# Performance work log

Hardware: AMD Instinct MI355X
Metric: run time of the kernel (lower is better)

## Reference

```python
import jax, jax.numpy as jnp
import numpy as np

N_NODES = 50000
N_EDGES = 800000
F_IN = 128
HID = 128
N_GRAPHS = 64
N_CLASSES = 40


def _seg_max(vals, idx, num_segments):
    out = jax.ops.segment_max(vals, idx, num_segments=num_segments)
    # PyG max-aggregation fills empty segments with 0
    return jnp.where(jnp.isfinite(out), out, jnp.zeros_like(out))


def _mr_conv(x, src, dst, W, b):
    # message: x_j - x_i gathered per edge; aggregate: scatter-max at dst
    diff = x[src] - x[dst]                      # [E, F]
    aggr = _seg_max(diff, dst, x.shape[0])      # [N, F]
    return jnp.concatenate([x, aggr], axis=-1) @ W + b


def setup_inputs() -> dict:
    key = jax.random.key(0)
    ks = jax.random.split(key, 16)
    x = jax.random.normal(ks[0], (N_NODES, F_IN), dtype=jnp.float32)
    edge_index = jax.random.randint(ks[1], (2, N_EDGES), 0, N_NODES, dtype=jnp.int64) if jax.config.jax_enable_x64 else jax.random.randint(ks[1], (2, N_EDGES), 0, N_NODES).astype(jnp.int32)
    batch = jnp.sort(jax.random.randint(ks[2], (N_NODES,), 0, N_GRAPHS)).astype(jnp.int32)
    def lin(k, fan_in, fan_out):
        bound = 1.0 / np.sqrt(fan_in)
        kw, kb = jax.random.split(k)
        W = jax.random.uniform(kw, (fan_in, fan_out), minval=-bound, maxval=bound, dtype=jnp.float32)
        b = jax.random.uniform(kb, (fan_out,), minval=-bound, maxval=bound, dtype=jnp.float32)
        return W, b
    W1, b1 = lin(ks[3], 2 * F_IN, HID)
    W2, b2 = lin(ks[4], 2 * HID, HID)
    W3, b3 = lin(ks[5], 2 * HID, HID)
    Wf1, bf1 = lin(ks[6], HID, 64)
    Wf2, bf2 = lin(ks[7], 64, N_CLASSES)
    return {"x": x, "edge_index": edge_index, "batch": batch,
            "W1": W1, "b1": b1, "W2": W2, "b2": b2, "W3": W3, "b3": b3,
            "Wf1": Wf1, "bf1": bf1, "Wf2": Wf2, "bf2": bf2}


def reference(x, edge_index, batch, W1, b1, W2, b2, W3, b3, Wf1, bf1, Wf2, bf2):
    src, dst = edge_index[0], edge_index[1]
    # to_undirected: add reversed edges (dedup unnecessary: max is idempotent)
    src_u = jnp.concatenate([src, dst])
    dst_u = jnp.concatenate([dst, src])
    h = _mr_conv(x, src_u, dst_u, W1, b1)
    h = jax.nn.relu(h)
    h = _mr_conv(h, src_u, dst_u, W2, b2)
    h = jax.nn.relu(h)
    h = _mr_conv(h, src_u, dst_u, W3, b3)
    h = jax.nn.relu(h)
    g = _seg_max(h, batch, N_GRAPHS)            # global_max_pool -> [G, HID]
    g = jax.nn.relu(g @ Wf1 + bf1) @ Wf2 + bf2
    return jax.nn.log_softmax(g, axis=1)
```

## Files before the change

### kernel.cpp

```cpp
#include <hip/hip_runtime.h>
#include <hip/hip_bf16.h>
#include <math.h>

#define NODES 50000
#define FEAT 128
#define NB 196
#define BCAP 12288

typedef __attribute__((ext_vector_type(4))) float f32x4;
typedef __attribute__((ext_vector_type(8))) short short8;
union UV { uint4 u; short8 s; };

__device__ __forceinline__ unsigned bf16rne(float x) {
  unsigned u = __float_as_uint(x);
  return (u + 0x7FFFu + ((u >> 16) & 1u)) >> 16;
}

__global__ void k_zero(int* __restrict__ p, int n) {
  int i = blockIdx.x * blockDim.x + threadIdx.x;
  if (i < n) p[i] = 0;
}

__global__ __launch_bounds__(256) void k_cast(const float* __restrict__ in,
                                              unsigned* __restrict__ out, int n2) {
  int i = blockIdx.x * 256 + threadIdx.x;
  if (i < n2) {
    float2 v = ((const float2*)in)[i];
    out[i] = bf16rne(v.x) | (bf16rne(v.y) << 16);
  }
}

__global__ __launch_bounds__(256) void k_wpack(const float* __restrict__ W,
                                               uint4* __restrict__ Wb) {
  int tid = blockIdx.x * 256 + threadIdx.x;
  int lane = tid & 63, nf = (tid >> 6) & 7, ks = tid >> 9;
  int kb = ks * 32 + (lane >> 4) * 8;
  int col = nf * 16 + (lane & 15);
  uint4 r;
  r.x = bf16rne(W[(kb + 0) * FEAT + col]) | (bf16rne(W[(kb + 1) * FEAT + col]) << 16);
  r.y = bf16rne(W[(kb + 2) * FEAT + col]) | (bf16rne(W[(kb + 3) * FEAT + col]) << 16);
  r.z = bf16rne(W[(kb + 4) * FEAT + col]) | (bf16rne(W[(kb + 5) * FEAT + col]) << 16);
  r.w = bf16rne(W[(kb + 6) * FEAT + col]) | (bf16rne(W[(kb + 7) * FEAT + col]) << 16);
  Wb[tid] = r;
}

__global__ __launch_bounds__(256) void k_bcount(const int* __restrict__ src,
                                                const int* __restrict__ dst,
                                                int E, int* __restrict__ bcount) {
  __shared__ int cnt[NB];
  int t = threadIdx.x;
  for (int i = t; i < NB; i += 256) cnt[i] = 0;
  __syncthreads();
  int base = blockIdx.x * 4096;
  int nE = min(4096, E - base);
  for (int k = t; k < nE; k += 256) {
    int s = src[base + k], d = dst[base + k];
    atomicAdd(&cnt[d >> 8], 1);
    atomicAdd(&cnt[s >> 8], 1);
  }
  __syncthreads();
  for (int i = t; i < NB; i += 256)
    if (cnt[i]) atomicAdd(&bcount[i], cnt[i]);
}

__global__ __launch_bounds__(256) void k_bscan(const int* __restrict__ bcount,
                                               int* __restrict__ bbase, int twoE) {
  __shared__ int sc[256];
  int t = threadIdx.x;
  int v = (t < NB) ? bcount[t] : 0;
  sc[t] = v;
  __syncthreads();
  for (int off = 1; off < 256; off <<= 1) {
    int u = (t >= off) ? sc[t - off] : 0;
    __syncthreads();
    sc[t] += u;
    __syncthreads();
  }
  if (t < NB) bbase[t] = sc[t] - v;
  if (t == 0) bbase[NB] = twoE;
}

__global__ __launch_bounds__(256) void k_bin(const int* __restrict__ src,
                                             const int* __restrict__ dst, int E,
                                             const int* __restrict__ bbase,
                                             int* __restrict__ bcur,
                                             uint2* __restrict__ binned) {
  __shared__ uint2 stage[8192];
  __shared__ int cnt[NB];
  __shared__ int lbase[NB];
  __shared__ int gbase[NB];
  __shared__ int lcur[NB];
  __shared__ int sc[256];
  int t = threadIdx.x;
  for (int i = t; i < NB; i += 256) cnt[i] = 0;
  __syncthreads();
  int base = blockIdx.x * 4096;
  int nE = min(4096, E - base);
  for (int k = t; k < nE; k += 256) {
    int s = src[base + k], d = dst[base + k];
    atomicAdd(&cnt[d >> 8], 1);
    atomicAdd(&cnt[s >> 8], 1);
  }
  __syncthreads();
  int v = (t < NB) ? cnt[t] : 0;
  sc[t] = v;
  __syncthreads();
  for (int off = 1; off < 256; off <<= 1) {
    int u = (t >= off) ? sc[t - off] : 0;
    __syncthreads();
    sc[t] += u;
    __syncthreads();
  }
  if (t < NB) {
    lbase[t] = sc[t] - v;
    lcur[t] = sc[t] - v;
  }
  __syncthreads();
  int total = sc[255];
  for (int k = t; k < nE; k += 256) {
    int s = src[base + k], d = dst[base + k];
    int p1 = atomicAdd(&lcur[d >> 8], 1);
    stage[p1] = make_uint2((unsigned)d, (unsigned)s);
    int p2 = atomicAdd(&lcur[s >> 8], 1);
    stage[p2] = make_uint2((unsigned)s, (unsigned)d);
  }
  __syncthreads();
  if (t < NB && cnt[t] > 0) gbase[t] = bbase[t] + atomicAdd(&bcur[t], cnt[t]);
  __syncthreads();
  for (int k = t; k < total; k += 256) {
    uint2 p = stage[k];
    int b = p.x >> 8;
    binned[gbase[b] + (k - lbase[b])] = p;
  }
}

__global__ __launch_bounds__(256) void k_build(const int* __restrict__ bbase,
                                               const uint2* __restrict__ binned,
                                               int* __restrict__ offs,
                                               int* __restrict__ adj,
                                               int N, int twoE) {
  __shared__ int hist[256];
  __shared__ int sc[256];
  __shared__ int lcur[256];
  __shared__ int adjS[BCAP];
  int b = blockIdx.x, t = threadIdx.x;
  int lo = bbase[b], hi = bbase[b + 1];
  int cntb = hi - lo;
  hist[t] = 0;
  __syncthreads();
  for (int k = t; k < cntb; k += 256) {
    uint2 p = binned[lo + k];
    atomicAdd(&hist[p.x & 255], 1);
  }
  __syncthreads();
  int v = hist[t];
  sc[t] = v;
  __syncthreads();
  for (int off = 1; off < 256; off <<= 1) {
    int u = (t >= off) ? sc[t - off] : 0;
    __syncthreads();
    sc[t] += u;
    __syncthreads();
  }
  int excl = sc[t] - v;
  lcur[t] = excl;
  int node = (b << 8) + t;
  if (node < N) offs[node] = lo + excl;
  if (b == NB - 1 && t == 0) offs[N] = twoE;
  __syncthreads();
  for (int k = t; k < cntb; k += 256) {
    uint2 p = binned[lo + k];
    int pos = atomicAdd(&lcur[p.x & 255], 1);
    adjS[pos] = (int)p.y;
  }
  __syncthreads();
  for (int k = t; k < cntb; k += 256) adj[lo + k] = adjS[k];
}

__global__ __launch_bounds__(256) void k_nmax(
    const unsigned* __restrict__ h16, const int* __restrict__ offs,
    const int* __restrict__ adj, unsigned* __restrict__ aggr16) {
  int i = blockIdx.x * 4 + (threadIdx.x >> 6);
  int lane = threadIdx.x & 63;
  int o0 = offs[i], o1 = offs[i + 1];
  float mlo0 = -INFINITY, mhi0 = -INFINITY;
  float mlo1 = -INFINITY, mhi1 = -INFINITY;
  int e = o0;
  for (; e + 4 <= o1; e += 4) {
    int j0 = adj[e], j1 = adj[e + 1], j2 = adj[e + 2], j3 = adj[e + 3];
    unsigned u0 = h16[(size_t)j0 * 64 + lane];
    unsigned u1 = h16[(size_t)j1 * 64 + lane];
    unsigned u2 = h16[(size_t)j2 * 64 + lane];
    unsigned u3 = h16[(size_t)j3 * 64 + lane];
    mlo0 = fmaxf(mlo0, __uint_as_float(u0 << 16));
    mhi0 = fmaxf(mhi0, __uint_as_float(u0 & 0xFFFF0000u));
    mlo1 = fmaxf(mlo1, __uint_as_float(u1 << 16));
    mhi1 = fmaxf(mhi1, __uint_as_float(u1 & 0xFFFF0000u));
    mlo0 = fmaxf(mlo0, __uint_as_float(u2 << 16));
    mhi0 = fmaxf(mhi0, __uint_as_float(u2 & 0xFFFF0000u));
    mlo1 = fmaxf(mlo1, __uint_as_float(u3 << 16));
    mhi1 = fmaxf(mhi1, __uint_as_float(u3 & 0xFFFF0000u));
  }
  for (; e < o1; ++e) {
    unsigned u0 = h16[(size_t)adj[e] * 64 + lane];
    mlo0 = fmaxf(mlo0, __uint_as_float(u0 << 16));
    mhi0 = fmaxf(mhi0, __uint_as_float(u0 & 0xFFFF0000u));
  }
  float mlo = fmaxf(mlo0, mlo1), mhi = fmaxf(mhi0, mhi1);
  unsigned us = h16[(size_t)i * 64 + lane];
  float hx = __uint_as_float(us << 16);
  float hy = __uint_as_float(us & 0xFFFF0000u);
  float rx = (o1 > o0) ? (mlo - hx) : 0.f;
  float ry = (o1 > o0) ? (mhi - hy) : 0.f;
  aggr16[(size_t)i * 64 + lane] = bf16rne(rx) | (bf16rne(ry) << 16);
}

__global__ __launch_bounds__(256) void k_gemm_mfma(
    const uint4* __restrict__ A1, const uint4* __restrict__ A2,
    const uint4* __restrict__ Wb, const float* __restrict__ bias,
    unsigned* __restrict__ out16, int N) {
  __shared__ uint4 Bs[4096];
  int t = threadIdx.x;
  int m0 = blockIdx.x * 64;
  for (int i = t; i < 4096; i += 256) Bs[i] = Wb[i];
  int wave = t >> 6, lane = t & 63;
  int kg = lane >> 4;
  int arow = m0 + wave * 16 + (lane & 15);
  int arc = min(arow, N - 1);
  const uint4* R1 = A1 + (size_t)arc * 16;
  const uint4* R2 = A2 + (size_t)arc * 16;
  f32x4 acc[8];
#pragma unroll
  for (int nf = 0; nf < 8; ++nf) acc[nf] = (f32x4){0.f, 0.f, 0.f, 0.f};
  __syncthreads();
#pragma unroll
  for (int ks = 0; ks < 8; ++ks) {
    UV a;
    a.u = (ks < 4) ? R1[ks * 4 + kg] : R2[(ks - 4) * 4 + kg];
#pragma unroll
    for (int nf = 0; nf < 8; ++nf) {
      UV b;
      b.u = Bs[(ks * 8 + nf) * 64 + lane];
      acc[nf] = __builtin_amdgcn_mfma_f32_16x16x32_bf16(a.s, b.s, acc[nf], 0, 0, 0);
    }
  }
  __syncthreads();
  unsigned short* Ct = (unsigned short*)Bs;
#pragma unroll
  for (int nf = 0; nf < 8; ++nf) {
    float bc = bias[nf * 16 + (lane & 15)];
#pragma unroll
    for (int r = 0; r < 4; ++r) {
      int row = wave * 16 + kg * 4 + r;
      float v = fmaxf(acc[nf][r] + bc, 0.f);
      Ct[row * 132 + nf * 16 + (lane & 15)] = (unsigned short)bf16rne(v);
    }
  }
  __syncthreads();
  const unsigned* CtU = (const unsigned*)Bs;
  for (int i = t; i < 4096; i += 256) {
    int row = i >> 6, cp = i & 63;
    int gr = m0 + row;
    if (gr < N) out16[(size_t)gr * 64 + cp] = CtU[row * 66 + cp];
  }
}

__global__ __launch_bounds__(64) void k_pool(
    const unsigned* __restrict__ h16, const int* __restrict__ batch,
    float* __restrict__ g, int N) {
  int f = threadIdx.x;
  int base = blockIdx.x * 64;
  int end = min(base + 64, N);
  int cur = -1;
  float mx = 0.f, my = 0.f;
  for (int n = base; n < end; ++n) {
    int b = batch[n];
    if (b != cur) {
      if (cur >= 0) {
        atomicMax((int*)&g[cur * FEAT + 2 * f], __float_as_int(mx));
        atomicMax((int*)&g[cur * FEAT + 2 * f + 1], __float_as_int(my));
      }
      cur = b;
      mx = my = 0.f;
    }
    unsigned u = h16[(size_t)n * 64 + f];
    mx = fmaxf(mx, __uint_as_float(u << 16));
    my = fmaxf(my, __uint_as_float(u & 0xFFFF0000u));
  }
  if (cur >= 0) {
    atomicMax((int*)&g[cur * FEAT + 2 * f], __float_as_int(mx));
    atomicMax((int*)&g[cur * FEAT + 2 * f + 1], __float_as_int(my));
  }
}

__global__ __launch_bounds__(64) void k_mlp(
    const float* __restrict__ g, const float* __restrict__ Wf1,
    const float* __restrict__ bf1, const float* __restrict__ Wf2,
    const float* __restrict__ bf2, float* __restrict__ out) {
  __shared__ float gr[128];
  __shared__ float h1[64];
  int gi = blockIdx.x, t = threadIdx.x;
  gr[t] = g[gi * FEAT + t];
  gr[t + 64] = g[gi * FEAT + 64 + t];
  __syncthreads();
  float acc = bf1[t];
#pragma unroll 4
  for (int k = 0; k < 128; ++k) acc += gr[k] * Wf1[k * 64 + t];
  h1[t] = fmaxf(acc, 0.f);
  __syncthreads();
  float logit = -INFINITY;
  if (t < 40) {
    float a = bf2[t];
#pragma unroll 4
    for (int k = 0; k < 64; ++k) a += h1[k] * Wf2[k * 40 + t];
    logit = a;
  }
  float m = logit;
#pragma unroll
  for (int off = 32; off; off >>= 1) m = fmaxf(m, __shfl_xor(m, off));
  float e = (t < 40) ? expf(logit - m) : 0.f;
  float s = e;
#pragma unroll
  for (int off = 32; off; off >>= 1) s += __shfl_xor(s, off);
  if (t < 40) out[gi * 40 + t] = logit - m - logf(s);
}

extern "C" void kernel_launch(void* const* d_in, const int* in_sizes, int n_in,
                              void* d_out, int out_size, void* d_ws, size_t ws_size,
                              hipStream_t stream) {
  const float* x = (const float*)d_in[0];
  const int* ei = (const int*)d_in[1];
  const int* batch = (const int*)d_in[2];
  const float* W1 = (const float*)d_in[3];
  const float* b1 = (const float*)d_in[4];
  const float* W2 = (const float*)d_in[5];
  const float* b2 = (const float*)d_in[6];
  const float* W3 = (const float*)d_in[7];
  const float* b3 = (const float*)d_in[8];
  const float* Wf1 = (const float*)d_in[9];
  const float* bf1 = (const float*)d_in[10];
  const float* Wf2 = (const float*)d_in[11];
  const float* bf2 = (const float*)d_in[12];
  float* out = (float*)d_out;

  const int N = NODES;
  const int E = in_sizes[1] / 2;
  const int* src = ei;
  const int* dst = ei + E;

  char* ws = (char*)d_ws;
  size_t off = 0;
  auto carve = [&](size_t bytes) {
    void* p = ws + off;
    off += (bytes + 255) & ~(size_t)255;
    return p;
  };
  unsigned* hA16 = (unsigned*)carve((size_t)N * 64 * 4);
  unsigned* hB16 = (unsigned*)carve((size_t)N * 64 * 4);
  unsigned* aggr16 = (unsigned*)carve((size_t)N * 64 * 4);
  uint4* Wb1 = (uint4*)carve(65536);
  uint4* Wb2 = (uint4*)carve(65536);
  uint4* Wb3 = (uint4*)carve(65536);
  int* zreg = (int*)carve((size_t)(256 + 256 + 64 * FEAT) * 4);
  int* bcount = zreg;
  int* bcur = zreg + 256;
  float* g = (float*)(zreg + 512);
  int* bbase = (int*)carve((size_t)(NB + 1) * 4);
  int* offs = (int*)carve((size_t)(N + 1) * 4);
  int* adj = (int*)carve((size_t)2 * E * 4);
  uint2* binned = (uint2*)aggr16;

  const int nzero = 256 + 256 + 64 * FEAT;
  const int nEB = (E + 4095) / 4096;
  const int nMB = (N + 63) / 64;

  k_zero<<<(nzero + 255) / 256, 256, 0, stream>>>(zreg, nzero);
  k_bcount<<<nEB, 256, 0, stream>>>(src, dst, E, bcount);
  k_bscan<<<1, 256, 0, stream>>>(bcount, bbase, 2 * E);
  k_bin<<<nEB, 256, 0, stream>>>(src, dst, E, bbase, bcur, binned);
  k_build<<<NB, 256, 0, stream>>>(bbase, binned, offs, adj, N, 2 * E);

  k_cast<<<(N * 64 + 255) / 256, 256, 0, stream>>>(x, hA16, N * 64);
  k_wpack<<<16, 256, 0, stream>>>(W1, Wb1);
  k_wpack<<<16, 256, 0, stream>>>(W2, Wb2);
  k_wpack<<<16, 256, 0, stream>>>(W3, Wb3);

  k_nmax<<<N / 4, 256, 0, stream>>>(hA16, offs, adj, aggr16);
  k_gemm_mfma<<<nMB, 256, 0, stream>>>((const uint4*)hA16, (const uint4*)aggr16, Wb1, b1, hB16, N);
  k_nmax<<<N / 4, 256, 0, stream>>>(hB16, offs, adj, aggr16);
  k_gemm_mfma<<<nMB, 256, 0, stream>>>((const uint4*)hB16, (const uint4*)aggr16, Wb2, b2, hA16, N);
  k_nmax<<<N / 4, 256, 0, stream>>>(hA16, offs, adj, aggr16);
  k_gemm_mfma<<<nMB, 256, 0, stream>>>((const uint4*)hA16, (const uint4*)aggr16, Wb3, b3, hB16, N);

  k_pool<<<(N + 63) / 64, 64, 0, stream>>>(hB16, batch, g, N);
  k_mlp<<<64, 64, 0, stream>>>(g, Wf1, bf1, Wf2, bf2, out);
}
```

Baseline: 417.5 us.

## Partition neighbor lists by source range and fuse pooling into final GEMM

The CSR build now splits each node's neighbor list into 8 partitions keyed by source-node range, producing per-partition offsets. The max-aggregation kernel has each wave handle 7 nodes and walk all nodes partition by partition, so concurrent gathers hit a narrower slice of the feature table and get better cache locality. Global max pooling is fused into the last GEMM epilogue, which skips writing the final hidden state, and the cast, weight-pack and zero kernels are merged into one launch. In exchange the offset array is 8x larger, each wave does more serial work, and the grid is much smaller, which can hurt latency hiding.

```diff
diff --git a/kernel.cpp b/kernel.cpp
--- a/kernel.cpp
+++ b/kernel.cpp
@@ -6,6 +6,7 @@
 #define FEAT 128
 #define NB 196
 #define BCAP 12288
+#define NPH 6250
 
 typedef __attribute__((ext_vector_type(4))) float f32x4;
 typedef __attribute__((ext_vector_type(8))) short short8;
@@ -16,32 +17,34 @@
   return (u + 0x7FFFu + ((u >> 16) & 1u)) >> 16;
 }
 
-__global__ void k_zero(int* __restrict__ p, int n) {
-  int i = blockIdx.x * blockDim.x + threadIdx.x;
-  if (i < n) p[i] = 0;
-}
-
-__global__ __launch_bounds__(256) void k_cast(const float* __restrict__ in,
-                                              unsigned* __restrict__ out, int n2) {
-  int i = blockIdx.x * 256 + threadIdx.x;
-  if (i < n2) {
-    float2 v = ((const float2*)in)[i];
-    out[i] = bf16rne(v.x) | (bf16rne(v.y) << 16);
-  }
-}
-
-__global__ __launch_bounds__(256) void k_wpack(const float* __restrict__ W,
-                                               uint4* __restrict__ Wb) {
-  int tid = blockIdx.x * 256 + threadIdx.x;
-  int lane = tid & 63, nf = (tid >> 6) & 7, ks = tid >> 9;
-  int kb = ks * 32 + (lane >> 4) * 8;
-  int col = nf * 16 + (lane & 15);
-  uint4 r;
-  r.x = bf16rne(W[(kb + 0) * FEAT + col]) | (bf16rne(W[(kb + 1) * FEAT + col]) << 16);
-  r.y = bf16rne(W[(kb + 2) * FEAT + col]) | (bf16rne(W[(kb + 3) * FEAT + col]) << 16);
-  r.z = bf16rne(W[(kb + 4) * FEAT + col]) | (bf16rne(W[(kb + 5) * FEAT + col]) << 16);
-  r.w = bf16rne(W[(kb + 6) * FEAT + col]) | (bf16rne(W[(kb + 7) * FEAT + col]) << 16);
-  Wb[tid] = r;
+__global__ __launch_bounds__(256) void k_prep(
+    const float* __restrict__ x, const float* __restrict__ W1,
+    const float* __restrict__ W2, const float* __restrict__ W3,
+    unsigned* __restrict__ h16, uint4* __restrict__ Wb1,
+    uint4* __restrict__ Wb2, uint4* __restrict__ Wb3, int* __restrict__ zreg) {
+  int b = blockIdx.x, t = threadIdx.x;
+  if (b < 12500) {
+    int i = b * 256 + t;
+    float2 v = ((const float2*)x)[i];
+    h16[i] = bf16rne(v.x) | (bf16rne(v.y) << 16);
+  } else if (b < 12548) {
+    int q = b - 12500;
+    const float* __restrict__ W = (q < 16) ? W1 : (q < 32) ? W2 : W3;
+    uint4* __restrict__ Wb = (q < 16) ? Wb1 : (q < 32) ? Wb2 : Wb3;
+    int tid = (q & 15) * 256 + t;
+    int lane = tid & 63, nf = (tid >> 6) & 7, ks = tid >> 9;
+    int kb = ks * 32 + (lane >> 4) * 8;
+    int col = nf * 16 + (lane & 15);
+    uint4 r;
+    r.x = bf16rne(W[(kb + 0) * FEAT + col]) | (bf16rne(W[(kb + 1) * FEAT + col]) << 16);
+    r.y = bf16rne(W[(kb + 2) * FEAT + col]) | (bf16rne(W[(kb + 3) * FEAT + col]) << 16);
+    r.z = bf16rne(W[(kb + 4) * FEAT + col]) | (bf16rne(W[(kb + 5) * FEAT + col]) << 16);
+    r.w = bf16rne(W[(kb + 6) * FEAT + col]) | (bf16rne(W[(kb + 7) * FEAT + col]) << 16);
+    Wb[tid] = r;
+  } else {
+    int i = (b - 12548) * 256 + t;
+    if (i < 8704) zreg[i] = 0;
+  }
 }
 
 __global__ __launch_bounds__(256) void k_bcount(const int* __restrict__ src,
@@ -136,25 +139,31 @@
 
 __global__ __launch_bounds__(256) void k_build(const int* __restrict__ bbase,
                                                const uint2* __restrict__ binned,
-                                               int* __restrict__ offs,
+                                               int* __restrict__ offs8,
                                                int* __restrict__ adj,
                                                int N, int twoE) {
-  __shared__ int hist[256];
+  __shared__ int hist[2048];
   __shared__ int sc[256];
-  __shared__ int lcur[256];
+  __shared__ int lcur[2048];
   __shared__ int adjS[BCAP];
   int b = blockIdx.x, t = threadIdx.x;
   int lo = bbase[b], hi = bbase[b + 1];
   int cntb = hi - lo;
-  hist[t] = 0;
+  for (int i = t; i < 2048; i += 256) hist[i] = 0;
   __syncthreads();
   for (int k = t; k < cntb; k += 256) {
     uint2 p = binned[lo + k];
-    atomicAdd(&hist[p.x & 255], 1);
-  }
-  __syncthreads();
-  int v = hist[t];
-  sc[t] = v;
+    atomicAdd(&hist[((p.x & 255) << 3) | (p.y / NPH)], 1);
+  }
+  __syncthreads();
+  int loc[8];
+  int run = 0;
+#pragma unroll
+  for (int j = 0; j < 8; ++j) {
+    loc[j] = run;
+    run += hist[(t << 3) | j];
+  }
+  sc[t] = run;
   __syncthreads();
   for (int off = 1; off < 256; off <<= 1) {
     int u = (t >= off) ? sc[t - off] : 0;
@@ -162,15 +171,19 @@
     sc[t] += u;
     __syncthreads();
   }
-  int excl = sc[t] - v;
-  lcur[t] = excl;
+  int excl0 = sc[t] - run;
   int node = (b << 8) + t;
-  if (node < N) offs[node] = lo + excl;
-  if (b == NB - 1 && t == 0) offs[N] = twoE;
+#pragma unroll
+  for (int j = 0; j < 8; ++j) {
+    int e = excl0 + loc[j];
+    lcur[(t << 3) | j] = e;
+    if (node < N) offs8[(size_t)node * 8 + j] = lo + e;
+  }
+  if (b == NB - 1 && t == 0) offs8[(size_t)N * 8] = twoE;
   __syncthreads();
   for (int k = t; k < cntb; k += 256) {
     uint2 p = binned[lo + k];
-    int pos = atomicAdd(&lcur[p.x & 255], 1);
+    int pos = atomicAdd(&lcur[((p.x & 255) << 3) | (p.y / NPH)], 1);
     adjS[pos] = (int)p.y;
   }
   __syncthreads();
@@ -178,47 +191,65 @@
 }
 
 __global__ __launch_bounds__(256) void k_nmax(
-    const unsigned* __restrict__ h16, const int* __restrict__ offs,
+    const unsigned* __restrict__ h16, const int* __restrict__ offs8,
     const int* __restrict__ adj, unsigned* __restrict__ aggr16) {
-  int i = blockIdx.x * 4 + (threadIdx.x >> 6);
+  int w = (blockIdx.x << 2) + (threadIdx.x >> 6);
   int lane = threadIdx.x & 63;
-  int o0 = offs[i], o1 = offs[i + 1];
-  float mlo0 = -INFINITY, mhi0 = -INFINITY;
-  float mlo1 = -INFINITY, mhi1 = -INFINITY;
-  int e = o0;
-  for (; e + 4 <= o1; e += 4) {
-    int j0 = adj[e], j1 = adj[e + 1], j2 = adj[e + 2], j3 = adj[e + 3];
-    unsigned u0 = h16[(size_t)j0 * 64 + lane];
-    unsigned u1 = h16[(size_t)j1 * 64 + lane];
-    unsigned u2 = h16[(size_t)j2 * 64 + lane];
-    unsigned u3 = h16[(size_t)j3 * 64 + lane];
-    mlo0 = fmaxf(mlo0, __uint_as_float(u0 << 16));
-    mhi0 = fmaxf(mhi0, __uint_as_float(u0 & 0xFFFF0000u));
-    mlo1 = fmaxf(mlo1, __uint_as_float(u1 << 16));
-    mhi1 = fmaxf(mhi1, __uint_as_float(u1 & 0xFFFF0000u));
-    mlo0 = fmaxf(mlo0, __uint_as_float(u2 << 16));
-    mhi0 = fmaxf(mhi0, __uint_as_float(u2 & 0xFFFF0000u));
-    mlo1 = fmaxf(mlo1, __uint_as_float(u3 << 16));
-    mhi1 = fmaxf(mhi1, __uint_as_float(u3 & 0xFFFF0000u));
-  }
-  for (; e < o1; ++e) {
-    unsigned u0 = h16[(size_t)adj[e] * 64 + lane];
-    mlo0 = fmaxf(mlo0, __uint_as_float(u0 << 16));
-    mhi0 = fmaxf(mhi0, __uint_as_float(u0 & 0xFFFF0000u));
-  }
-  float mlo = fmaxf(mlo0, mlo1), mhi = fmaxf(mhi0, mhi1);
-  unsigned us = h16[(size_t)i * 64 + lane];
-  float hx = __uint_as_float(us << 16);
-  float hy = __uint_as_float(us & 0xFFFF0000u);
-  float rx = (o1 > o0) ? (mlo - hx) : 0.f;
-  float ry = (o1 > o0) ? (mhi - hy) : 0.f;
-  aggr16[(size_t)i * 64 + lane] = bf16rne(rx) | (bf16rne(ry) << 16);
+  float ml[7], mh[7];
+#pragma unroll
+  for (int k = 0; k < 7; ++k) {
+    ml[k] = -INFINITY;
+    mh[k] = -INFINITY;
+  }
+  for (int p = 0; p < 8; ++p) {
+#pragma unroll
+    for (int k = 0; k < 7; ++k) {
+      int i = w + (k << 13);
+      if (i < NODES) {
+        int s = offs8[(size_t)i * 8 + p];
+        int e = offs8[(size_t)i * 8 + p + 1];
+        float a = ml[k], c = mh[k];
+        int q = s;
+        for (; q + 2 <= e; q += 2) {
+          int j0 = adj[q], j1 = adj[q + 1];
+          unsigned u0 = h16[(size_t)j0 * 64 + lane];
+          unsigned u1 = h16[(size_t)j1 * 64 + lane];
+          a = fmaxf(a, __uint_as_float(u0 << 16));
+          c = fmaxf(c, __uint_as_float(u0 & 0xFFFF0000u));
+          a = fmaxf(a, __uint_as_float(u1 << 16));
+          c = fmaxf(c, __uint_as_float(u1 & 0xFFFF0000u));
+        }
+        if (q < e) {
+          unsigned u0 = h16[(size_t)adj[q] * 64 + lane];
+          a = fmaxf(a, __uint_as_float(u0 << 16));
+          c = fmaxf(c, __uint_as_float(u0 & 0xFFFF0000u));
+        }
+        ml[k] = a;
+        mh[k] = c;
+      }
+    }
+  }
+#pragma unroll
+  for (int k = 0; k < 7; ++k) {
+    int i = w + (k << 13);
+    if (i < NODES) {
+      int d0 = offs8[(size_t)i * 8];
+      int d1 = offs8[(size_t)i * 8 + 8];
+      unsigned us = h16[(size_t)i * 64 + lane];
+      float hx = __uint_as_float(us << 16);
+      float hy = __uint_as_float(us & 0xFFFF0000u);
+      float rx = (d1 > d0) ? (ml[k] - hx) : 0.f;
+      float ry = (d1 > d0) ? (mh[k] - hy) : 0.f;
+      aggr16[(size_t)i * 64 + lane] = bf16rne(rx) | (bf16rne(ry) << 16);
+    }
+  }
 }
 
 __global__ __launch_bounds__(256) void k_gemm_mfma(
     const uint4* __restrict__ A1, const uint4* __restrict__ A2,
     const uint4* __restrict__ Wb, const float* __restrict__ bias,
-    unsigned* __restrict__ out16, int N) {
+    unsigned* __restrict__ out16, const int* __restrict__ batch,
+    float* __restrict__ g, int N) {
   __shared__ uint4 Bs[4096];
   int t = threadIdx.x;
   int m0 = blockIdx.x * 64;
@@ -257,39 +288,30 @@
     }
   }
   __syncthreads();
-  const unsigned* CtU = (const unsigned*)Bs;
-  for (int i = t; i < 4096; i += 256) {
-    int row = i >> 6, cp = i & 63;
-    int gr = m0 + row;
-    if (gr < N) out16[(size_t)gr * 64 + cp] = CtU[row * 66 + cp];
-  }
-}
-
-__global__ __launch_bounds__(64) void k_pool(
-    const unsigned* __restrict__ h16, const int* __restrict__ batch,
-    float* __restrict__ g, int N) {
-  int f = threadIdx.x;
-  int base = blockIdx.x * 64;
-  int end = min(base + 64, N);
-  int cur = -1;
-  float mx = 0.f, my = 0.f;
-  for (int n = base; n < end; ++n) {
-    int b = batch[n];
-    if (b != cur) {
-      if (cur >= 0) {
-        atomicMax((int*)&g[cur * FEAT + 2 * f], __float_as_int(mx));
-        atomicMax((int*)&g[cur * FEAT + 2 * f + 1], __float_as_int(my));
+  if (out16) {
+    const unsigned* CtU = (const unsigned*)Bs;
+    for (int i = t; i < 4096; i += 256) {
+      int row = i >> 6, cp = i & 63;
+      int gr = m0 + row;
+      if (gr < N) out16[(size_t)gr * 64 + cp] = CtU[row * 66 + cp];
+    }
+  } else if (t < 128) {
+    int f = t;
+    int cur = -1;
+    float m = 0.f;
+    for (int r = 0; r < 64; ++r) {
+      int gr = m0 + r;
+      if (gr >= N) break;
+      int bb = batch[gr];
+      if (bb != cur) {
+        if (cur >= 0) atomicMax((int*)&g[cur * FEAT + f], __float_as_int(m));
+        cur = bb;
+        m = 0.f;
       }
-      cur = b;
-      mx = my = 0.f;
-    }
-    unsigned u = h16[(size_t)n * 64 + f];
-    mx = fmaxf(mx, __uint_as_float(u << 16));
-    my = fmaxf(my, __uint_as_float(u & 0xFFFF0000u));
-  }
-  if (cur >= 0) {
-    atomicMax((int*)&g[cur * FEAT + 2 * f], __float_as_int(mx));
-    atomicMax((int*)&g[cur * FEAT + 2 * f + 1], __float_as_int(my));
+      unsigned u = (unsigned)Ct[r * 132 + f];
+      m = fmaxf(m, __uint_as_float(u << 16));
+    }
+    if (cur >= 0) atomicMax((int*)&g[cur * FEAT + f], __float_as_int(m));
   }
 }
 
@@ -361,37 +383,33 @@
   uint4* Wb1 = (uint4*)carve(65536);
   uint4* Wb2 = (uint4*)carve(65536);
   uint4* Wb3 = (uint4*)carve(65536);
-  int* zreg = (int*)carve((size_t)(256 + 256 + 64 * FEAT) * 4);
+  int* zreg = (int*)carve((size_t)8704 * 4);
   int* bcount = zreg;
   int* bcur = zreg + 256;
   float* g = (float*)(zreg + 512);
   int* bbase = (int*)carve((size_t)(NB + 1) * 4);
-  int* offs = (int*)carve((size_t)(N + 1) * 4);
+  int* offs8 = (int*)carve(((size_t)N * 8 + 1) * 4);
   int* adj = (int*)carve((size_t)2 * E * 4);
   uint2* binned = (uint2*)aggr16;
 
-  const int nzero = 256 + 256 + 64 * FEAT;
   const int nEB = (E + 4095) / 4096;
   const int nMB = (N + 63) / 64;
 
-  k_zero<<<(nzero + 255) / 256, 256, 0, stream>>>(zreg, nzero);
+  k_prep<<<12582, 256, 0, stream>>>(x, W1, W2, W3, hA16, Wb1, Wb2, Wb3, zreg);
   k_bcount<<<nEB, 256, 0, stream>>>(src, dst, E, bcount);
   k_bscan<<<1, 256, 0, stream>>>(bcount, bbase, 2 * E);
   k_bin<<<nEB, 256, 0, stream>>>(src, dst, E, bbase, bcur, binned);
-  k_build<<<NB, 256, 0, stream>>>(bbase, binned, offs, adj, N, 2 * E);
-
-  k_cast<<<(N * 64 + 255) / 256, 256, 0, stream>>>(x, hA16, N * 64);
-  k_wpack<<<16, 256, 0, stream>>>(W1, Wb1);
-  k_wpack<<<16, 256, 0, stream>>>(W2, Wb2);
-  k_wpack<<<16, 256, 0, stream>>>(W3, Wb3);
-
-  k_nmax<<<N / 4, 256, 0, stream>>>(hA16, offs, adj, aggr16);
-  k_gemm_mfma<<<nMB, 256, 0, stream>>>((const uint4*)hA16, (const uint4*)aggr16, Wb1, b1, hB16, N);
-  k_nmax<<<N / 4, 256, 0, stream>>>(hB16, offs, adj, aggr16);
-  k_gemm_mfma<<<nMB, 256, 0, stream>>>((const uint4*)hB16, (const uint4*)aggr16, Wb2, b2, hA16, N);
-  k_nmax<<<N / 4, 256, 0, stream>>>(hA16, offs, adj, aggr16);
-  k_gemm_mfma<<<nMB, 256, 0, stream>>>((const uint4*)hA16, (const uint4*)aggr16, Wb3, b3, hB16, N);
-
-  k_pool<<<(N + 63) / 64, 64, 0, stream>>>(hB16, batch, g, N);
+  k_build<<<NB, 256, 0, stream>>>(bbase, binned, offs8, adj, N, 2 * E);
+
+  k_nmax<<<2048, 256, 0, stream>>>(hA16, offs8, adj, aggr16);
+  k_gemm_mfma<<<nMB, 256, 0, stream>>>((const uint4*)hA16, (const uint4*)aggr16,
+                                       Wb1, b1, hB16, batch, g, N);
+  k_nmax<<<2048, 256, 0, stream>>>(hB16, offs8, adj, aggr16);
+  k_gemm_mfma<<<nMB, 256, 0, stream>>>((const uint4*)hB16, (const uint4*)aggr16,
+                                       Wb2, b2, hA16, batch, g, N);
+  k_nmax<<<2048, 256, 0, stream>>>(hA16, offs8, adj, aggr16);
+  k_gemm_mfma<<<nMB, 256, 0, stream>>>((const uint4*)hA16, (const uint4*)aggr16,
+                                       Wb3, b3, (unsigned*)nullptr, batch, g, N);
+
   k_mlp<<<64, 64, 0, stream>>>(g, Wf1, bf1, Wf2, bf2, out);
 }
```

After: 516.1 us. 23.6% more time.
